# Kernel optimization log

Hardware: AMD Instinct MI355X
Metric: run time of the kernel (lower is better)

## Reference

```python
import jax, jax.numpy as jnp
import numpy as np

N = 50000        # nodes
N_EDGES = 800000 # edges before self loops
D_IN = 128       # in_features
D_OUT = 64       # out_features (per head)
H = 2            # heads
NEG_SLOPE = 0.2  # GATv2Conv default negative_slope
EPS = 1e-5       # LayerNorm eps


def setup_inputs() -> dict:
    key = jax.random.key(0)
    ks = jax.random.split(key, 8)
    X = jax.random.normal(ks[0], (N, D_IN), jnp.float32)
    E = jax.random.randint(ks[1], (2, N_EDGES), 0, N, dtype=jnp.int32)
    attr = jax.random.normal(ks[2], (N_EDGES,), jnp.float32)
    # GATv2Conv params: lin_l / lin_r (share_weights=False, bias=True), att, concat bias
    s_in = 1.0 / np.sqrt(D_IN)
    W_l = jax.random.normal(ks[3], (D_IN, H * D_OUT), jnp.float32) * s_in
    b_l = jnp.zeros((H * D_OUT,), jnp.float32)
    W_r = jax.random.normal(ks[4], (D_IN, H * D_OUT), jnp.float32) * s_in
    b_r = jnp.zeros((H * D_OUT,), jnp.float32)
    att = jax.random.normal(ks[5], (H, D_OUT), jnp.float32) * (1.0 / np.sqrt(D_OUT))
    bias = jnp.zeros((H * D_OUT,), jnp.float32)
    # final_linear + LayerNorm params
    W_f = jax.random.normal(ks[6], (H * D_OUT, D_OUT), jnp.float32) * (1.0 / np.sqrt(H * D_OUT))
    b_f = jnp.zeros((D_OUT,), jnp.float32)
    gamma = jnp.ones((D_OUT,), jnp.float32)
    beta = jnp.zeros((D_OUT,), jnp.float32)
    return dict(X=X, E=E, attr=attr, W_l=W_l, b_l=b_l, W_r=W_r, b_r=b_r,
                att=att, bias=bias, W_f=W_f, b_f=b_f, gamma=gamma, beta=beta)


def _forward(X, E, W_l, b_l, W_r, b_r, att, bias, W_f, b_f, gamma, beta):
    # add self loops (PyG GATv2Conv default add_self_loops=True)
    loop = jnp.arange(N, dtype=E.dtype)
    src = jnp.concatenate([E[0], loop])  # [Et]
    dst = jnp.concatenate([E[1], loop])  # [Et]
    x_l = (X @ W_l + b_l).reshape(N, H, D_OUT)  # source-side transform
    x_r = (X @ W_r + b_r).reshape(N, H, D_OUT)  # target-side transform
    # per-edge GATv2 score: a^T LeakyReLU(x_i + x_j)
    s = jax.nn.leaky_relu(x_l[src] + x_r[dst], NEG_SLOPE)      # [Et, H, C]
    alpha = jnp.einsum('ehc,hc->eh', s, att)                   # [Et, H]
    # segment softmax over incoming edges of each target node
    a_max = jax.ops.segment_max(alpha, dst, num_segments=N)    # [N, H]
    a_max = jnp.where(jnp.isfinite(a_max), a_max, 0.0)
    num = jnp.exp(alpha - a_max[dst])
    den = jax.ops.segment_sum(num, dst, num_segments=N)
    w = num / den[dst]                                         # [Et, H]
    # weighted scatter-aggregate of source messages
    out = jax.ops.segment_sum(x_l[src] * w[:, :, None], dst, num_segments=N)  # [N,H,C]
    out = out.reshape(N, H * D_OUT) + bias                     # concat heads + bias
    # final linear + LayerNorm
    h = out @ W_f + b_f                                        # [N, D_OUT]
    mu = jnp.mean(h, axis=-1, keepdims=True)
    var = jnp.mean((h - mu) ** 2, axis=-1, keepdims=True)
    return (h - mu) * jax.lax.rsqrt(var + EPS) * gamma + beta


def reference(X, E, attr, W_l, b_l, W_r, b_r, att, bias, W_f, b_f, gamma, beta):
    H_out = _forward(X, E, W_l, b_l, W_r, b_r, att, bias, W_f, b_f, gamma, beta)
    return (H_out, E, attr)
```

## Files before the change

kernel.cpp:

```cpp
#include <hip/hip_runtime.h>

typedef unsigned short u16;
typedef unsigned int   u32;


#define DIN   128
#define DOUT  64
#define HD    128
#define BCAP  64

typedef __attribute__((ext_vector_type(8))) _Float16 f16x8;
typedef __attribute__((ext_vector_type(2))) _Float16 h2;
typedef __attribute__((ext_vector_type(4))) float    f32x4;

union H2U { u32 u; h2 h; };
__device__ __forceinline__ h2  U2H(u32 u) { H2U x; x.u = u; return x.h; }
__device__ __forceinline__ u32 H2Ub(h2 h) { H2U x; x.h = h; return x.u; }

__device__ __forceinline__ u16 f2h(float f) {
    _Float16 h = (_Float16)f;
    u16 r; __builtin_memcpy(&r, &h, 2); return r;
}

__device__ __forceinline__ u32 pkmax(u32 a, u32 b) {
    u32 d;
    asm("v_pk_max_f16 %0, %1, %2" : "=v"(d) : "v"(a), "v"(b));
    return d;
}

__device__ __forceinline__ float fdot2f(h2 a, h2 b, float c) {
#if __has_builtin(__builtin_amdgcn_fdot2)
    return __builtin_amdgcn_fdot2(a, b, c, false);
#else
    return c + (float)a[0] * (float)b[0] + (float)a[1] * (float)b[1];
#endif
}

__global__ void prep_small(const float* __restrict__ Wl, const float* __restrict__ Wr,
                           const float* __restrict__ Wf,
                           u16* __restrict__ WTl, u16* __restrict__ WTr,
                           uint4* __restrict__ Wfp, int* __restrict__ count, int N)
{
    int i = blockIdx.x * 256 + threadIdx.x;
    if (i < N) { count[i] = 0; return; }
    int j = i - N;
    if (j < 16384) {
        int k = j >> 7, c = j & 127;
        WTl[c * 128 + k] = f2h(Wl[j]);
    } else if (j < 32768) {
        int t = j - 16384;
        int k = t >> 7, c = t & 127;
        WTr[c * 128 + k] = f2h(Wr[t]);
    } else if (j < 33792) {
        int t = j - 32768;
        int k4 = t >> 5, c = t & 31;
        const float* wrow = Wf + (size_t)(4 * k4) * DOUT;
        u32 a0 = (u32)f2h(wrow[c])              | ((u32)f2h(wrow[DOUT + c]) << 16);
        u32 a1 = (u32)f2h(wrow[2 * DOUT + c])   | ((u32)f2h(wrow[3 * DOUT + c]) << 16);
        u32 a2 = (u32)f2h(wrow[c + 32])         | ((u32)f2h(wrow[DOUT + c + 32]) << 16);
        u32 a3 = (u32)f2h(wrow[2 * DOUT + c + 32]) | ((u32)f2h(wrow[3 * DOUT + c + 32]) << 16);
        Wfp[t] = make_uint4(a0, a1, a2, a3);
    }
}

__global__ void edge_prep(const int* __restrict__ E, const float* __restrict__ attr,
                          int* __restrict__ count, u16* __restrict__ bucket,
                          float* __restrict__ out, int N, int NE)
{
    int i = blockIdx.x * 256 + threadIdx.x;
    if (i < NE) {
        int src = E[i];
        int dst = E[NE + i];
        if ((u32)dst >= (u32)N) dst = 0;
        if ((u32)src >= (u32)N) src = 0;
        int rank = atomicAdd(&count[dst], 1);
        if (rank < BCAP) bucket[(size_t)dst * BCAP + rank] = (u16)src;
    } else {
        int j = i - NE;
        const size_t base = (size_t)N * DOUT;
        if (j < 2 * NE) {
            out[base + j] = (float)E[j];
        } else {
            int t = j - 2 * NE;
            if (t < NE) out[base + 2 * (size_t)NE + t] = attr[t];
        }
    }
}

__global__ __launch_bounds__(256) void gemm1(
    const float* __restrict__ X,
    const u16* __restrict__ WTl, const float* __restrict__ bl,
    const u16* __restrict__ WTr, const float* __restrict__ br,
    u16* __restrict__ xl_p, u16* __restrict__ xr_p, int N)
{
    __shared__ u16 sX[64 * 136];
    __shared__ u16 sW[128 * 136];

    const int tid  = threadIdx.x;
    const int row0 = blockIdx.x * 64;
    const int cb   = blockIdx.y;
    const u16*   WT  = (cb == 0) ? WTl : WTr;
    const float* bia = (cb == 0) ? bl : br;

    for (int idx = tid; idx < 64 * 32; idx += 256) {
        int r  = idx >> 5;
        int k4 = (idx & 31) << 2;
        int gr = row0 + r;
        float4 v = make_float4(0.f, 0.f, 0.f, 0.f);
        if (gr < N) v = *(const float4*)(X + (size_t)gr * DIN + k4);
        u32 p0 = (u32)f2h(v.x) | ((u32)f2h(v.y) << 16);
        u32 p1 = (u32)f2h(v.z) | ((u32)f2h(v.w) << 16);
        *(uint2*)&sX[r * 136 + k4] = make_uint2(p0, p1);
    }
    for (int idx = tid; idx < 128 * 16; idx += 256) {
        int c  = idx >> 4;
        int k8 = (idx & 15) << 3;
        *(uint4*)&sW[c * 136 + k8] = *(const uint4*)&WT[c * 128 + k8];
    }
    __syncthreads();

    const int wv   = tid >> 6;
    const int lane = tid & 63;
    const int m    = lane & 15;
    const int quad = lane >> 4;

    f32x4 acc[8] = {};
    #pragma unroll
    for (int kc = 0; kc < 4; kc++) {
        f16x8 bx = *(const f16x8*)&sX[(wv * 16 + m) * 136 + kc * 32 + quad * 8];
        #pragma unroll
        for (int t = 0; t < 8; t++) {
            f16x8 aw = *(const f16x8*)&sW[(t * 16 + m) * 136 + kc * 32 + quad * 8];
            acc[t] = __builtin_amdgcn_mfma_f32_16x16x32_f16(aw, bx, acc[t], 0, 0, 0);
        }
    }

    const int gn = row0 + wv * 16 + m;
    if (gn < N) {
        u16* dst = (cb == 0) ? xl_p : xr_p;
        #pragma unroll
        for (int t = 0; t < 8; t++) {
            const int c0 = t * 16 + quad * 4;
            float4 bv = *(const float4*)(bia + c0);
            u32 p0 = (u32)f2h(acc[t][0] + bv.x) | ((u32)f2h(acc[t][1] + bv.y) << 16);
            u32 p1 = (u32)f2h(acc[t][2] + bv.z) | ((u32)f2h(acc[t][3] + bv.w) << 16);
            *(uint2*)(dst + (size_t)gn * HD + c0) = make_uint2(p0, p1);
        }
    }
}

template<int D>
__device__ __forceinline__ void edge_block(
    int myidx, int j, int sgbase, const char* xbase,
    const h2* xr2, const h2* at2, h2 c02,
    h2* acc2, float& lden)
{
    uint4 q[D];
    #pragma unroll
    for (int b = 0; b < D; b++) {
        u32 off = (u32)__shfl(myidx, sgbase + j + 2 * b) << 8;
        q[b] = *(const uint4*)(xbase + off);
    }
    float sh[D];
    #pragma unroll
    for (int b = 0; b < D; b++) {
        h2 v0 = U2H(q[b].x) + xr2[0];
        h2 v1 = U2H(q[b].y) + xr2[1];
        h2 v2 = U2H(q[b].z) + xr2[2];
        h2 v3 = U2H(q[b].w) + xr2[3];
        v0 = U2H(pkmax(H2Ub(v0), H2Ub(v0 * c02)));
        v1 = U2H(pkmax(H2Ub(v1), H2Ub(v1 * c02)));
        v2 = U2H(pkmax(H2Ub(v2), H2Ub(v2 * c02)));
        v3 = U2H(pkmax(H2Ub(v3), H2Ub(v3 * c02)));
        float s = fdot2f(v0, at2[0], 0.f);
        s = fdot2f(v1, at2[1], s);
        s = fdot2f(v2, at2[2], s);
        s = fdot2f(v3, at2[3], s);
        sh[b] = s;
    }
    #pragma unroll
    for (int m = 4; m; m >>= 1) {
        #pragma unroll
        for (int b = 0; b < D; b++) sh[b] += __shfl_xor(sh[b], m);
    }
    #pragma unroll
    for (int b = 0; b < D; b++) {
        float p = exp2f(sh[b]);
        lden += p;
        _Float16 ph = (_Float16)p;
        h2 p2 = {ph, ph};
        acc2[0] += p2 * U2H(q[b].x);
        acc2[1] += p2 * U2H(q[b].y);
        acc2[2] += p2 * U2H(q[b].z);
        acc2[3] += p2 * U2H(q[b].w);
    }
}

__global__ __launch_bounds__(256, 8) void edge_fused(
    const u16* __restrict__ xl_p, const u16* __restrict__ xr_p,
    const float* __restrict__ att, const float* __restrict__ bias,
    const uint4* __restrict__ Wfp, const float* __restrict__ bf,
    const float* __restrict__ gamma, const float* __restrict__ beta,
    const int* __restrict__ count, const u16* __restrict__ bucket,
    float* __restrict__ out, int N)
{
    __shared__ uint4 sWp[32 * 32];
    __shared__ u32   sAggU[8 * 64];

    const int tid = threadIdx.x;
    for (int idx = tid; idx < 1024; idx += 256) sWp[idx] = Wfp[idx];
    __syncthreads();

    const int l      = tid & 63;
    const int half   = tid >> 5;
    const int hl     = tid & 31;
    const int g16    = l & 15;
    const int ch0    = g16 * 8;
    const int sgsel  = (l >> 4) & 1;
    const int sgbase = (l & 32) + sgsel;
    const int n      = blockIdx.x * 8 + half;
    const bool active = (n < N);

    const h2 c02 = {(_Float16)0.2f, (_Float16)0.2f};
    h2 at2[4], xr2[4];
    {
        const float L2E = 1.44269504f;
        float4 a0 = *(const float4*)(att + ch0);
        float4 a1 = *(const float4*)(att + ch0 + 4);
        at2[0] = h2{(_Float16)(a0.x * L2E), (_Float16)(a0.y * L2E)};
        at2[1] = h2{(_Float16)(a0.z * L2E), (_Float16)(a0.w * L2E)};
        at2[2] = h2{(_Float16)(a1.x * L2E), (_Float16)(a1.y * L2E)};
        at2[3] = h2{(_Float16)(a1.z * L2E), (_Float16)(a1.w * L2E)};
        uint4 pr = make_uint4(0, 0, 0, 0);
        if (active) pr = *(const uint4*)(xr_p + (size_t)n * HD + ch0);
        xr2[0] = U2H(pr.x); xr2[1] = U2H(pr.y);
        xr2[2] = U2H(pr.z); xr2[3] = U2H(pr.w);
    }

    h2 acc2[4] = {};
    float lden = 0.f;

    int cnt_b = 0;
    if (active) {
        cnt_b = count[n];
        if (cnt_b < 0) cnt_b = 0;
        if (cnt_b > BCAP) cnt_b = BCAP;
    }
    const int cnt = active ? cnt_b + 1 : 0;
    const u16* mybkt = bucket + (size_t)(active ? n : 0) * BCAP;

    const char* xbase = (const char*)xl_p + ch0 * 2;

    int done = 0;
    while (done < cnt) {
        int chunk = cnt - done; if (chunk > 32) chunk = 32;
        int myidx = 0;
        if (hl < chunk) {
            int gj = done + hl;
            myidx = (gj < cnt_b) ? (int)mybkt[gj] : n;
        }
        int j = 0;
        for (; j + 16 <= chunk; j += 16)
            edge_block<8>(myidx, j, sgbase, xbase, xr2, at2, c02, acc2, lden);
        if (j + 8 <= chunk) {
            edge_block<4>(myidx, j, sgbase, xbase, xr2, at2, c02, acc2, lden);
            j += 8;
        }
        if (j + 4 <= chunk) {
            edge_block<2>(myidx, j, sgbase, xbase, xr2, at2, c02, acc2, lden);
            j += 4;
        }
        for (; j < chunk; j += 2) {
            u32 off = (u32)__shfl(myidx, sgbase + j) << 8;
            uint4 q = *(const uint4*)(xbase + off);
            h2 v0 = U2H(q.x) + xr2[0];
            h2 v1 = U2H(q.y) + xr2[1];
            h2 v2 = U2H(q.z) + xr2[2];
            h2 v3 = U2H(q.w) + xr2[3];
            v0 = U2H(pkmax(H2Ub(v0), H2Ub(v0 * c02)));
            v1 = U2H(pkmax(H2Ub(v1), H2Ub(v1 * c02)));
            v2 = U2H(pkmax(H2Ub(v2), H2Ub(v2 * c02)));
            v3 = U2H(pkmax(H2Ub(v3), H2Ub(v3 * c02)));
            float s = fdot2f(v0, at2[0], 0.f);
            s = fdot2f(v1, at2[1], s);
            s = fdot2f(v2, at2[2], s);
            s = fdot2f(v3, at2[3], s);
            #pragma unroll
            for (int m = 4; m; m >>= 1) s += __shfl_xor(s, m);
            float p = (j + sgsel < chunk) ? exp2f(s) : 0.f;
            lden += p;
            _Float16 ph = (_Float16)p;
            h2 p2 = {ph, ph};
            acc2[0] += p2 * U2H(q.x);
            acc2[1] += p2 * U2H(q.y);
            acc2[2] += p2 * U2H(q.z);
            acc2[3] += p2 * U2H(q.w);
        }
        done += chunk;
    }

    #pragma unroll
    for (int i = 0; i < 4; i++) {
        u32 o = (u32)__shfl_xor((int)H2Ub(acc2[i]), 16);
        acc2[i] = acc2[i] + U2H(o);
    }
    lden += __shfl_xor(lden, 16);

    float rl = 1.f / fmaxf(lden, 1e-30f);
    if (!(l & 16)) {
        float4 b0 = *(const float4*)(bias + ch0);
        float4 b1 = *(const float4*)(bias + ch0 + 4);
        uint4 w;
        w.x = (u32)f2h((float)acc2[0][0] * rl + b0.x) |
              ((u32)f2h((float)acc2[0][1] * rl + b0.y) << 16);
        w.y = (u32)f2h((float)acc2[1][0] * rl + b0.z) |
              ((u32)f2h((float)acc2[1][1] * rl + b0.w) << 16);
        w.z = (u32)f2h((float)acc2[2][0] * rl + b1.x) |
              ((u32)f2h((float)acc2[2][1] * rl + b1.y) << 16);
        w.w = (u32)f2h((float)acc2[3][0] * rl + b1.z) |
              ((u32)f2h((float)acc2[3][1] * rl + b1.w) << 16);
        *(uint4*)&sAggU[half * 64 + g16 * 4] = w;
    }
    asm volatile("s_waitcnt lgkmcnt(0)" ::: "memory");

    float h0 = bf[hl], h1 = bf[hl + 32];
    #pragma unroll 8
    for (int k4 = 0; k4 < 32; k4++) {
        uint4 wp = sWp[k4 * 32 + hl];
        uint2 ag = *(const uint2*)&sAggU[half * 64 + k4 * 2];
        h0 = fdot2f(U2H(ag.x), U2H(wp.x), h0);
        h0 = fdot2f(U2H(ag.y), U2H(wp.y), h0);
        h1 = fdot2f(U2H(ag.x), U2H(wp.z), h1);
        h1 = fdot2f(U2H(ag.y), U2H(wp.w), h1);
    }

    float s1r = h0 + h1, s2r = h0 * h0 + h1 * h1;
    #pragma unroll
    for (int m = 16; m; m >>= 1) { s1r += __shfl_xor(s1r, m); s2r += __shfl_xor(s2r, m); }
    float mu  = s1r * (1.f / 64.f);
    float var = s2r * (1.f / 64.f) - mu * mu;
    float rs  = rsqrtf(fmaxf(var, 0.f) + 1e-5f);
    if (active) {
        out[(size_t)n * DOUT + hl]      = (h0 - mu) * rs * gamma[hl]      + beta[hl];
        out[(size_t)n * DOUT + hl + 32] = (h1 - mu) * rs * gamma[hl + 32] + beta[hl + 32];
    }
}

extern "C" void kernel_launch(void* const* d_in, const int* in_sizes, int n_in,
                              void* d_out, int out_size, void* d_ws, size_t ws_size,
                              hipStream_t stream) {
    const float* X    = (const float*)d_in[0];
    const int*   E    = (const int*)d_in[1];
    const float* attr = (const float*)d_in[2];
    const float* Wl   = (const float*)d_in[3];
    const float* bl   = (const float*)d_in[4];
    const float* Wr   = (const float*)d_in[5];
    const float* br   = (const float*)d_in[6];
    const float* att  = (const float*)d_in[7];
    const float* bias = (const float*)d_in[8];
    const float* Wf   = (const float*)d_in[9];
    const float* bf   = (const float*)d_in[10];
    const float* gamma= (const float*)d_in[11];
    const float* beta = (const float*)d_in[12];
    float* out = (float*)d_out;

    const int N  = in_sizes[0] / DIN;
    const int NE = in_sizes[1] / 2;

    char* ws = (char*)d_ws;
    int* count      = (int*)ws;               ws += (size_t)N * 4;
    u16* bucket     = (u16*)ws;               ws += (size_t)N * BCAP * 2;
    u16* xl_p       = (u16*)ws;               ws += (size_t)N * HD * 2;
    u16* xr_p       = (u16*)ws;               ws += (size_t)N * HD * 2;
    u16* WTl        = (u16*)ws;               ws += 128 * 128 * 2;
    u16* WTr        = (u16*)ws;               ws += 128 * 128 * 2;
    uint4* Wfp      = (uint4*)ws;             ws += 1024 * 16;

    prep_small<<<(N + 33792 + 255) / 256, 256, 0, stream>>>(
        Wl, Wr, Wf, WTl, WTr, Wfp, count, N);

    edge_prep<<<(4 * NE + 255) / 256, 256, 0, stream>>>(
        E, attr, count, bucket, out, N, NE);

    gemm1<<<dim3((N + 63) / 64, 2), 256, 0, stream>>>(X, WTl, bl, WTr, br, xl_p, xr_p, N);

    edge_fused<<<(N + 7) / 8, 256, 0, stream>>>(
        xl_p, xr_p, att, bias, Wfp, bf, gamma, beta,
        count, bucket, out, N);
}
```

Before: 223.1 us.

## Fuse edge bucketing and passthrough copy into the projection GEMM kernel

Removes the separate edge_prep launch and folds its work into the GEMM kernel. Each GEMM block first processes a contiguous slice of edges (atomic bucket insertion) and a slice of the E/attr passthrough copy, then does its 64-row tile of the projection. This saves a launch and lets the memory-bound scatter overlap with GEMM compute across blocks, but it serialises the scatter ahead of the GEMM inside each block. The edge_fused launch bound also drops from 8 to 6 waves per SIMD, giving the compiler more registers at the cost of occupancy.

```diff
diff --git a/kernel.cpp b/kernel.cpp
--- a/kernel.cpp
+++ b/kernel.cpp
@@ -63,44 +63,46 @@
     }
 }
 
-__global__ void edge_prep(const int* __restrict__ E, const float* __restrict__ attr,
-                          int* __restrict__ count, u16* __restrict__ bucket,
-                          float* __restrict__ out, int N, int NE)
-{
-    int i = blockIdx.x * 256 + threadIdx.x;
-    if (i < NE) {
-        int src = E[i];
-        int dst = E[NE + i];
-        if ((u32)dst >= (u32)N) dst = 0;
-        if ((u32)src >= (u32)N) src = 0;
-        int rank = atomicAdd(&count[dst], 1);
-        if (rank < BCAP) bucket[(size_t)dst * BCAP + rank] = (u16)src;
-    } else {
-        int j = i - NE;
-        const size_t base = (size_t)N * DOUT;
-        if (j < 2 * NE) {
-            out[base + j] = (float)E[j];
-        } else {
-            int t = j - 2 * NE;
-            if (t < NE) out[base + 2 * (size_t)NE + t] = attr[t];
-        }
-    }
-}
-
-__global__ __launch_bounds__(256) void gemm1(
+__global__ __launch_bounds__(256) void gemm_scatter(
     const float* __restrict__ X,
     const u16* __restrict__ WTl, const float* __restrict__ bl,
     const u16* __restrict__ WTr, const float* __restrict__ br,
-    u16* __restrict__ xl_p, u16* __restrict__ xr_p, int N)
+    const int* __restrict__ E, const float* __restrict__ attr,
+    int* __restrict__ count, u16* __restrict__ bucket,
+    u16* __restrict__ xl_p, u16* __restrict__ xr_p,
+    float* __restrict__ out, int N, int NE)
 {
     __shared__ u16 sX[64 * 136];
     __shared__ u16 sW[128 * 136];
 
     const int tid  = threadIdx.x;
-    const int row0 = blockIdx.x * 64;
-    const int cb   = blockIdx.y;
+    const int bid  = blockIdx.x;
+    const int nB   = gridDim.x;
+    const int cb   = bid & 1;
+    const int row0 = (bid >> 1) * 64;
     const u16*   WT  = (cb == 0) ? WTl : WTr;
     const float* bia = (cb == 0) ? bl : br;
+
+    {
+        int e0 = (int)(((long long)bid) * NE / nB);
+        int e1 = (int)(((long long)bid + 1) * NE / nB);
+        for (int e = e0 + tid; e < e1; e += 256) {
+            int src = E[e];
+            int dst = E[NE + e];
+            if ((u32)dst >= (u32)N) dst = 0;
+            if ((u32)src >= (u32)N) src = 0;
+            int rank = atomicAdd(&count[dst], 1);
+            if (rank < BCAP) bucket[(size_t)dst * BCAP + rank] = (u16)src;
+        }
+        const size_t base = (size_t)N * DOUT;
+        long long P = 3LL * NE;
+        int p0 = (int)(((long long)bid) * P / nB);
+        int p1 = (int)(((long long)bid + 1) * P / nB);
+        for (int p = p0 + tid; p < p1; p += 256) {
+            if (p < 2 * NE) out[base + p] = (float)E[p];
+            else            out[base + p] = attr[p - 2 * NE];
+        }
+    }
 
     for (int idx = tid; idx < 64 * 32; idx += 256) {
         int r  = idx >> 5;
@@ -196,7 +198,7 @@
     }
 }
 
-__global__ __launch_bounds__(256, 8) void edge_fused(
+__global__ __launch_bounds__(256, 6) void edge_fused(
     const u16* __restrict__ xl_p, const u16* __restrict__ xr_p,
     const float* __restrict__ att, const float* __restrict__ bias,
     const uint4* __restrict__ Wfp, const float* __restrict__ bf,
@@ -366,6 +368,7 @@
 
     const int N  = in_sizes[0] / DIN;
     const int NE = in_sizes[1] / 2;
+    const int GB = (N + 63) / 64;
 
     char* ws = (char*)d_ws;
     int* count      = (int*)ws;               ws += (size_t)N * 4;
@@ -379,10 +382,8 @@
     prep_small<<<(N + 33792 + 255) / 256, 256, 0, stream>>>(
         Wl, Wr, Wf, WTl, WTr, Wfp, count, N);
 
-    edge_prep<<<(4 * NE + 255) / 256, 256, 0, stream>>>(
-        E, attr, count, bucket, out, N, NE);
-
-    gemm1<<<dim3((N + 63) / 64, 2), 256, 0, stream>>>(X, WTl, bl, WTr, br, xl_p, xr_p, N);
+    gemm_scatter<<<2 * GB, 256, 0, stream>>>(
+        X, WTl, bl, WTr, br, E, attr, count, bucket, xl_p, xr_p, out, N, NE);
 
     edge_fused<<<(N + 7) / 8, 256, 0, stream>>>(
         xl_p, xr_p, att, bias, Wfp, bf, gamma, beta,
```

Result: faster. 215.8 us (-3.3%).
